# Optimization experiments

Hardware: AMD Instinct MI355X
Metric: run time of the kernel (lower is better)

Reference implementation:

```python
import jax, jax.numpy as jnp
import numpy as np

N = 500000      # total nodes
B = 10000       # number of graphs
D = 256         # node_size == global_size
SLOPE = 0.01    # LeakyReLU negative slope (torch default)

def leaky_relu(x):
    return jnp.where(x >= 0, x, SLOPE * x)

def setup_inputs() -> dict:
    key = jax.random.key(0)
    ks = jax.random.split(key, 10)
    xg_old = jax.random.normal(ks[0], (B, D), dtype=jnp.float32)
    x = jax.random.normal(ks[1], (N, D), dtype=jnp.float32)
    batch = jnp.sort(jax.random.randint(ks[2], (N,), 0, B)).astype(jnp.int64)
    s = 1.0 / np.sqrt(D)
    W_gate = jax.random.uniform(ks[3], (D, 1), minval=-s, maxval=s, dtype=jnp.float32)
    b_gate = jax.random.uniform(ks[4], (1,), minval=-s, maxval=s, dtype=jnp.float32)
    W_feat = jax.random.uniform(ks[5], (D, D), minval=-s, maxval=s, dtype=jnp.float32)
    b_feat = jax.random.uniform(ks[6], (D,), minval=-s, maxval=s, dtype=jnp.float32)
    s2 = 1.0 / np.sqrt(2 * D)
    W_t = jax.random.uniform(ks[7], (2 * D, D), minval=-s2, maxval=s2, dtype=jnp.float32)
    b_t = jax.random.uniform(ks[8], (D,), minval=-s2, maxval=s2, dtype=jnp.float32)
    return {"xg_old": xg_old, "x": x, "batch": batch,
            "W_gate": W_gate, "b_gate": b_gate,
            "W_feat": W_feat, "b_feat": b_feat,
            "W_t": W_t, "b_t": b_t}

def reference(xg_old, x, batch, W_gate, b_gate, W_feat, b_feat, W_t, b_t):
    batch = batch.astype(jnp.int32)
    # AttentionalAggregation: per-graph softmax over gate scores, weighted sum of feats
    gate = x @ W_gate + b_gate                               # [N, 1]
    feat = leaky_relu(x @ W_feat + b_feat)                   # [N, D]
    m = jax.ops.segment_max(gate, batch, num_segments=B)     # [B, 1]
    g = jnp.exp(gate - m[batch])                             # stable exp
    s = jax.ops.segment_sum(g, batch, num_segments=B)        # [B, 1]
    alpha = g / s[batch]                                     # [N, 1]
    xg = jax.ops.segment_sum(alpha * feat, batch, num_segments=B)  # [B, D]
    # concat with old global state, transform, residual
    cat = jnp.concatenate([xg, xg_old], axis=1)              # [B, 2D]
    out = leaky_relu(cat @ W_t + b_t) + xg_old               # [B, D]
    return out
```

## Files before the change

kernel.cpp:

```cpp
#include <hip/hip_runtime.h>
#include <hip/hip_bf16.h>
#include <math.h>

#define D 256

typedef short v8s __attribute__((ext_vector_type(8)));
typedef float f32x4 __attribute__((ext_vector_type(4)));

__global__ void segstart_kernel(const int* __restrict__ batch, int* __restrict__ seg_start,
                                int N, int B) {
    int b = blockIdx.x * blockDim.x + threadIdx.x;
    if (b > B) return;
    int lo = 0, hi = N;
    while (lo < hi) {
        int mid = (lo + hi) >> 1;
        if (batch[mid] < b) lo = mid + 1; else hi = mid;
    }
    seg_start[b] = lo;
}

__global__ __launch_bounds__(256) void gate_kernel(const float* __restrict__ x,
                                                   const float* __restrict__ Wg,
                                                   const float* __restrict__ bg,
                                                   float* __restrict__ gate, int N) {
    int wave = threadIdx.x >> 6;
    int lane = threadIdx.x & 63;
    int n = blockIdx.x * 4 + wave;
    if (n >= N) return;
    const float4 xv = *(const float4*)(x + (size_t)n * D + lane * 4);
    const float4 wv = *(const float4*)(Wg + lane * 4);
    float d = xv.x * wv.x + xv.y * wv.y + xv.z * wv.z + xv.w * wv.w;
    #pragma unroll
    for (int off = 32; off > 0; off >>= 1) d += __shfl_down(d, off, 64);
    if (lane == 0) gate[n] = d + bg[0];
}

__global__ __launch_bounds__(256) void stats_kernel(const float* __restrict__ gate,
                                                    const int* __restrict__ seg_start,
                                                    float* __restrict__ mvec,
                                                    float* __restrict__ invs, int B) {
    int wid = blockIdx.x * 4 + (threadIdx.x >> 6);
    int lane = threadIdx.x & 63;
    if (wid >= B) return;
    int s0 = seg_start[wid], s1 = seg_start[wid + 1];
    float m = -INFINITY;
    for (int i = s0 + lane; i < s1; i += 64) m = fmaxf(m, gate[i]);
    #pragma unroll
    for (int off = 32; off > 0; off >>= 1) m = fmaxf(m, __shfl_xor(m, off, 64));
    float s = 0.f;
    for (int i = s0 + lane; i < s1; i += 64) s += __expf(gate[i] - m);
    #pragma unroll
    for (int off = 32; off > 0; off >>= 1) s += __shfl_xor(s, off, 64);
    if (lane == 0) { mvec[wid] = m; invs[wid] = (s > 0.f) ? 1.f / s : 0.f; }
}

__global__ void wconv_kernel(const float* __restrict__ Wf, unsigned short* __restrict__ Wb) {
    int idx = blockIdx.x * 256 + threadIdx.x;
    int k = idx >> 8, n = idx & 255;
    int n_tile = n >> 4, k_step = k >> 5;
    int lane = ((k >> 3) & 3) * 16 + (n & 15);
    int j = k & 7;
    int dst = (((n_tile * 8 + k_step) * 64) + lane) * 8 + j;
    Wb[dst] = __bfloat16_as_ushort(__float2bfloat16(Wf[k * 256 + n]));
}

__global__ __launch_bounds__(256) void feat_attn_kernel(
    const float* __restrict__ x, const unsigned short* __restrict__ Wb,
    const float* __restrict__ bfeat, const float* __restrict__ gate,
    const int* __restrict__ batch, const float* __restrict__ mvec,
    const float* __restrict__ invs, float* __restrict__ xg, int N) {

    __shared__ unsigned short feat_s[64 * 260];
    __shared__ float alpha_s[64];
    __shared__ int batch_s[64];

    const int tid = threadIdx.x;
    const int n0 = blockIdx.x * 64;
    const int cnt = min(64, N - n0);

    if (tid < 64) {
        if (tid < cnt) {
            int n = n0 + tid;
            int b = batch[n];
            batch_s[tid] = b;
            alpha_s[tid] = __expf(gate[n] - mvec[b]) * invs[b];
        } else { batch_s[tid] = -1; alpha_s[tid] = 0.f; }
    }

    const int w = tid >> 6, lane = tid & 63;
    const int mrow = lane & 15, q = lane >> 4;

    f32x4 acc[4][4];
    #pragma unroll
    for (int i = 0; i < 4; i++)
        #pragma unroll
        for (int j = 0; j < 4; j++) acc[i][j] = (f32x4){0.f, 0.f, 0.f, 0.f};

    size_t rowbase[4];
    #pragma unroll
    for (int rb = 0; rb < 4; rb++) {
        int r = n0 + rb * 16 + mrow;
        if (r > N - 1) r = N - 1;
        rowbase[rb] = (size_t)r * D + q * 8;
    }

    for (int ks = 0; ks < 8; ks++) {
        v8s a[4], bfr[4];
        #pragma unroll
        for (int rb = 0; rb < 4; rb++) {
            const float* p = x + rowbase[rb] + ks * 32;
            float4 f0 = *(const float4*)p;
            float4 f1 = *(const float4*)(p + 4);
            v8s v;
            v[0] = (short)__bfloat16_as_ushort(__float2bfloat16(f0.x));
            v[1] = (short)__bfloat16_as_ushort(__float2bfloat16(f0.y));
            v[2] = (short)__bfloat16_as_ushort(__float2bfloat16(f0.z));
            v[3] = (short)__bfloat16_as_ushort(__float2bfloat16(f0.w));
            v[4] = (short)__bfloat16_as_ushort(__float2bfloat16(f1.x));
            v[5] = (short)__bfloat16_as_ushort(__float2bfloat16(f1.y));
            v[6] = (short)__bfloat16_as_ushort(__float2bfloat16(f1.z));
            v[7] = (short)__bfloat16_as_ushort(__float2bfloat16(f1.w));
            a[rb] = v;
        }
        #pragma unroll
        for (int cb = 0; cb < 4; cb++) {
            int nt = w * 4 + cb;
            bfr[cb] = *(const v8s*)(Wb + (((size_t)nt * 8 + ks) * 64 + lane) * 8);
        }
        #pragma unroll
        for (int rb = 0; rb < 4; rb++)
            #pragma unroll
            for (int cb = 0; cb < 4; cb++)
                acc[rb][cb] = __builtin_amdgcn_mfma_f32_16x16x32_bf16(
                    a[rb], bfr[cb], acc[rb][cb], 0, 0, 0);
    }

    #pragma unroll
    for (int cb = 0; cb < 4; cb++) {
        int col = w * 64 + cb * 16 + mrow;
        float bias = bfeat[col];
        #pragma unroll
        for (int rb = 0; rb < 4; rb++) {
            #pragma unroll
            for (int reg = 0; reg < 4; reg++) {
                float y = acc[rb][cb][reg] + bias;
                y = (y >= 0.f) ? y : 0.01f * y;
                feat_s[(rb * 16 + q * 4 + reg) * 260 + col] =
                    __bfloat16_as_ushort(__float2bfloat16(y));
            }
        }
    }
    __syncthreads();

    float sum = 0.f;
    int cur = batch_s[0];
    for (int i = 0; i < cnt; i++) {
        int b = batch_s[i];
        if (b != cur) {
            atomicAdd(&xg[(size_t)cur * D + tid], sum);
            sum = 0.f; cur = b;
        }
        float y = __bfloat162float(__ushort_as_bfloat16(feat_s[i * 260 + tid]));
        sum = fmaf(alpha_s[i], y, sum);
    }
    atomicAdd(&xg[(size_t)cur * D + tid], sum);
}

__global__ __launch_bounds__(256) void out_kernel(
    const float* __restrict__ xg, const float* __restrict__ xg_old,
    const float* __restrict__ Wt, const float* __restrict__ bt,
    float* __restrict__ out) {
    const int t = threadIdx.x;
    const int r0 = blockIdx.x * 8;
    float acc[8];
    #pragma unroll
    for (int r = 0; r < 8; r++) acc[r] = 0.f;

    for (int k = 0; k < D; k++) {
        const float w = Wt[k * D + t];
        #pragma unroll
        for (int r = 0; r < 8; r++)
            acc[r] = fmaf(xg[(size_t)(r0 + r) * D + k], w, acc[r]);
    }
    for (int k = 0; k < D; k++) {
        const float w = Wt[(D + k) * D + t];
        #pragma unroll
        for (int r = 0; r < 8; r++)
            acc[r] = fmaf(xg_old[(size_t)(r0 + r) * D + k], w, acc[r]);
    }
    const float btt = bt[t];
    #pragma unroll
    for (int r = 0; r < 8; r++) {
        float y = acc[r] + btt;
        y = (y >= 0.f) ? y : 0.01f * y;
        out[(size_t)(r0 + r) * D + t] = y + xg_old[(size_t)(r0 + r) * D + t];
    }
}

extern "C" void kernel_launch(void* const* d_in, const int* in_sizes, int n_in,
                              void* d_out, int out_size, void* d_ws, size_t ws_size,
                              hipStream_t stream) {
    const float* xg_old = (const float*)d_in[0];
    const float* x      = (const float*)d_in[1];
    const int*   batch  = (const int*)d_in[2];
    const float* W_gate = (const float*)d_in[3];
    const float* b_gate = (const float*)d_in[4];
    const float* W_feat = (const float*)d_in[5];
    const float* b_feat = (const float*)d_in[6];
    const float* W_t    = (const float*)d_in[7];
    const float* b_t    = (const float*)d_in[8];
    float* out = (float*)d_out;

    const int N = in_sizes[1] / D;
    const int B = in_sizes[0] / D;

    char* ws = (char*)d_ws;
    int*            seg_start = (int*)ws;
    float*          gate      = (float*)(ws + 0x10000);
    float*          mvec      = (float*)(ws + 0x220000);
    float*          invs      = (float*)(ws + 0x230000);
    unsigned short* Wb        = (unsigned short*)(ws + 0x240000);
    float*          xg        = (float*)(ws + 0x280000);

    segstart_kernel<<<(B + 1 + 255) / 256, 256, 0, stream>>>(batch, seg_start, N, B);
    gate_kernel<<<(N + 3) / 4, 256, 0, stream>>>(x, W_gate, b_gate, gate, N);
    stats_kernel<<<(B + 3) / 4, 256, 0, stream>>>(gate, seg_start, mvec, invs, B);
    wconv_kernel<<<256, 256, 0, stream>>>(W_feat, Wb);
    hipMemsetAsync(xg, 0, (size_t)B * D * sizeof(float), stream);
    feat_attn_kernel<<<(N + 63) / 64, 256, 0, stream>>>(
        x, Wb, b_feat, gate, batch, mvec, invs, xg, N);
    out_kernel<<<B / 8, 256, 0, stream>>>(xg, xg_old, W_t, b_t, out);
}
```

Measured before the change: 1.106 ms.

## Pre-convert x to bf16 in gate pass and use MFMA for output transform

The gate kernel becomes a grid-stride loop that also writes a bf16 copy of x, so the feature GEMM can read half the bytes instead of re-reading fp32 x. The output transform is rewritten to use bf16 MFMA, working on a bf16 concat buffer and a pre-swizzled W_t, replacing the scalar FMA loop. This adds an extra write of a bf16 copy of x (N*D*2 bytes) plus conversion kernels, and lowers the precision of the final GEMM. Both paths are gated on workspace size, with the old code kept as a fallback.

New measurement: 988.0 us. 10.7% less time.

```diff
diff --git a/kernel.cpp b/kernel.cpp
--- a/kernel.cpp
+++ b/kernel.cpp
@@ -6,6 +6,10 @@
 
 typedef short v8s __attribute__((ext_vector_type(8)));
 typedef float f32x4 __attribute__((ext_vector_type(4)));
+
+__device__ __forceinline__ unsigned short f2b(float f) {
+    return __bfloat16_as_ushort(__float2bfloat16(f));
+}
 
 __global__ void segstart_kernel(const int* __restrict__ batch, int* __restrict__ seg_start,
                                 int N, int B) {
@@ -19,20 +23,27 @@
     seg_start[b] = lo;
 }
 
-__global__ __launch_bounds__(256) void gate_kernel(const float* __restrict__ x,
-                                                   const float* __restrict__ Wg,
-                                                   const float* __restrict__ bg,
-                                                   float* __restrict__ gate, int N) {
-    int wave = threadIdx.x >> 6;
-    int lane = threadIdx.x & 63;
-    int n = blockIdx.x * 4 + wave;
-    if (n >= N) return;
-    const float4 xv = *(const float4*)(x + (size_t)n * D + lane * 4);
+template<bool CONV>
+__global__ __launch_bounds__(256) void gate_conv_kernel(
+    const float* __restrict__ x, const float* __restrict__ Wg,
+    const float* __restrict__ bg, float* __restrict__ gate,
+    unsigned short* __restrict__ xb16, int N) {
+    const int lane = threadIdx.x & 63;
+    const int wid = blockIdx.x * 4 + (threadIdx.x >> 6);
+    const int nw = gridDim.x * 4;
     const float4 wv = *(const float4*)(Wg + lane * 4);
-    float d = xv.x * wv.x + xv.y * wv.y + xv.z * wv.z + xv.w * wv.w;
-    #pragma unroll
-    for (int off = 32; off > 0; off >>= 1) d += __shfl_down(d, off, 64);
-    if (lane == 0) gate[n] = d + bg[0];
+    const float bgv = bg[0];
+    for (int n = wid; n < N; n += nw) {
+        const float4 xv = *(const float4*)(x + (size_t)n * D + lane * 4);
+        if (CONV) {
+            ushort4 h = { f2b(xv.x), f2b(xv.y), f2b(xv.z), f2b(xv.w) };
+            *(ushort4*)(xb16 + (size_t)n * D + lane * 4) = h;
+        }
+        float d = xv.x * wv.x + xv.y * wv.y + xv.z * wv.z + xv.w * wv.w;
+        #pragma unroll
+        for (int off = 32; off; off >>= 1) d += __shfl_xor(d, off, 64);
+        if (lane == 0) gate[n] = d + bgv;
+    }
 }
 
 __global__ __launch_bounds__(256) void stats_kernel(const float* __restrict__ gate,
@@ -54,18 +65,22 @@
     if (lane == 0) { mvec[wid] = m; invs[wid] = (s > 0.f) ? 1.f / s : 0.f; }
 }
 
-__global__ void wconv_kernel(const float* __restrict__ Wf, unsigned short* __restrict__ Wb) {
+__global__ void wconv_kernel(const float* __restrict__ Wf, unsigned short* __restrict__ Wb,
+                             int K) {
     int idx = blockIdx.x * 256 + threadIdx.x;
     int k = idx >> 8, n = idx & 255;
-    int n_tile = n >> 4, k_step = k >> 5;
+    if (k >= K) return;
+    int n_tile = n >> 4, k_step = k >> 5, ksteps = K >> 5;
     int lane = ((k >> 3) & 3) * 16 + (n & 15);
     int j = k & 7;
-    int dst = (((n_tile * 8 + k_step) * 64) + lane) * 8 + j;
-    Wb[dst] = __bfloat16_as_ushort(__float2bfloat16(Wf[k * 256 + n]));
-}
-
+    int dst = (((n_tile * ksteps + k_step) * 64) + lane) * 8 + j;
+    Wb[dst] = f2b(Wf[k * 256 + n]);
+}
+
+template<bool BF16IN>
 __global__ __launch_bounds__(256) void feat_attn_kernel(
-    const float* __restrict__ x, const unsigned short* __restrict__ Wb,
+    const float* __restrict__ x, const unsigned short* __restrict__ xb16,
+    const unsigned short* __restrict__ Wb,
     const float* __restrict__ bfeat, const float* __restrict__ gate,
     const int* __restrict__ batch, const float* __restrict__ mvec,
     const float* __restrict__ invs, float* __restrict__ xg, int N) {
@@ -108,19 +123,19 @@
         v8s a[4], bfr[4];
         #pragma unroll
         for (int rb = 0; rb < 4; rb++) {
-            const float* p = x + rowbase[rb] + ks * 32;
-            float4 f0 = *(const float4*)p;
-            float4 f1 = *(const float4*)(p + 4);
-            v8s v;
-            v[0] = (short)__bfloat16_as_ushort(__float2bfloat16(f0.x));
-            v[1] = (short)__bfloat16_as_ushort(__float2bfloat16(f0.y));
-            v[2] = (short)__bfloat16_as_ushort(__float2bfloat16(f0.z));
-            v[3] = (short)__bfloat16_as_ushort(__float2bfloat16(f0.w));
-            v[4] = (short)__bfloat16_as_ushort(__float2bfloat16(f1.x));
-            v[5] = (short)__bfloat16_as_ushort(__float2bfloat16(f1.y));
-            v[6] = (short)__bfloat16_as_ushort(__float2bfloat16(f1.z));
-            v[7] = (short)__bfloat16_as_ushort(__float2bfloat16(f1.w));
-            a[rb] = v;
+            if (BF16IN) {
+                a[rb] = *(const v8s*)(xb16 + rowbase[rb] + ks * 32);
+            } else {
+                const float* p = x + rowbase[rb] + ks * 32;
+                float4 f0 = *(const float4*)p;
+                float4 f1 = *(const float4*)(p + 4);
+                v8s v;
+                v[0] = (short)f2b(f0.x); v[1] = (short)f2b(f0.y);
+                v[2] = (short)f2b(f0.z); v[3] = (short)f2b(f0.w);
+                v[4] = (short)f2b(f1.x); v[5] = (short)f2b(f1.y);
+                v[6] = (short)f2b(f1.z); v[7] = (short)f2b(f1.w);
+                a[rb] = v;
+            }
         }
         #pragma unroll
         for (int cb = 0; cb < 4; cb++) {
@@ -145,8 +160,7 @@
             for (int reg = 0; reg < 4; reg++) {
                 float y = acc[rb][cb][reg] + bias;
                 y = (y >= 0.f) ? y : 0.01f * y;
-                feat_s[(rb * 16 + q * 4 + reg) * 260 + col] =
-                    __bfloat16_as_ushort(__float2bfloat16(y));
+                feat_s[(rb * 16 + q * 4 + reg) * 260 + col] = f2b(y);
             }
         }
     }
@@ -166,6 +180,76 @@
     atomicAdd(&xg[(size_t)cur * D + tid], sum);
 }
 
+__global__ void catconv_kernel(const float* __restrict__ xg, const float* __restrict__ xg_old,
+                               unsigned short* __restrict__ catb, int B) {
+    int idx = blockIdx.x * 256 + threadIdx.x;
+    if (idx >= B * 64) return;
+    int b = idx >> 6, c = (idx & 63) * 4;
+    float4 v1 = *(const float4*)(xg + (size_t)b * D + c);
+    float4 v2 = *(const float4*)(xg_old + (size_t)b * D + c);
+    ushort4 h1 = { f2b(v1.x), f2b(v1.y), f2b(v1.z), f2b(v1.w) };
+    ushort4 h2 = { f2b(v2.x), f2b(v2.y), f2b(v2.z), f2b(v2.w) };
+    *(ushort4*)(catb + (size_t)b * 512 + c) = h1;
+    *(ushort4*)(catb + (size_t)b * 512 + 256 + c) = h2;
+}
+
+__global__ __launch_bounds__(256) void out_mfma_kernel(
+    const unsigned short* __restrict__ catb, const unsigned short* __restrict__ Wtb,
+    const float* __restrict__ bt, const float* __restrict__ xg_old,
+    float* __restrict__ out, int B) {
+    const int tid = threadIdx.x;
+    const int w = tid >> 6, lane = tid & 63, mrow = lane & 15, q = lane >> 4;
+    const int r0 = blockIdx.x * 64;
+
+    f32x4 acc[4][4];
+    #pragma unroll
+    for (int i = 0; i < 4; i++)
+        #pragma unroll
+        for (int j = 0; j < 4; j++) acc[i][j] = (f32x4){0.f, 0.f, 0.f, 0.f};
+
+    size_t rowbase[4];
+    #pragma unroll
+    for (int rb = 0; rb < 4; rb++) {
+        int r = r0 + rb * 16 + mrow;
+        if (r > B - 1) r = B - 1;
+        rowbase[rb] = (size_t)r * 512 + q * 8;
+    }
+
+    for (int ks = 0; ks < 16; ks++) {
+        v8s a[4], bfr[4];
+        #pragma unroll
+        for (int rb = 0; rb < 4; rb++)
+            a[rb] = *(const v8s*)(catb + rowbase[rb] + ks * 32);
+        #pragma unroll
+        for (int cb = 0; cb < 4; cb++)
+            bfr[cb] = *(const v8s*)(Wtb + (((size_t)(w * 4 + cb) * 16 + ks) * 64 + lane) * 8);
+        #pragma unroll
+        for (int rb = 0; rb < 4; rb++)
+            #pragma unroll
+            for (int cb = 0; cb < 4; cb++)
+                acc[rb][cb] = __builtin_amdgcn_mfma_f32_16x16x32_bf16(
+                    a[rb], bfr[cb], acc[rb][cb], 0, 0, 0);
+    }
+
+    #pragma unroll
+    for (int cb = 0; cb < 4; cb++) {
+        int col = w * 64 + cb * 16 + mrow;
+        float bias = bt[col];
+        #pragma unroll
+        for (int rb = 0; rb < 4; rb++) {
+            #pragma unroll
+            for (int reg = 0; reg < 4; reg++) {
+                int row = r0 + rb * 16 + q * 4 + reg;
+                if (row < B) {
+                    float y = acc[rb][cb][reg] + bias;
+                    y = (y >= 0.f) ? y : 0.01f * y;
+                    out[(size_t)row * D + col] = y + xg_old[(size_t)row * D + col];
+                }
+            }
+        }
+    }
+}
+
 __global__ __launch_bounds__(256) void out_kernel(
     const float* __restrict__ xg, const float* __restrict__ xg_old,
     const float* __restrict__ Wt, const float* __restrict__ bt,
@@ -175,7 +259,6 @@
     float acc[8];
     #pragma unroll
     for (int r = 0; r < 8; r++) acc[r] = 0.f;
-
     for (int k = 0; k < D; k++) {
         const float w = Wt[k * D + t];
         #pragma unroll
@@ -220,14 +303,37 @@
     float*          mvec      = (float*)(ws + 0x220000);
     float*          invs      = (float*)(ws + 0x230000);
     unsigned short* Wb        = (unsigned short*)(ws + 0x240000);
-    float*          xg        = (float*)(ws + 0x280000);
+    unsigned short* Wtb       = (unsigned short*)(ws + 0x260000);
+    float*          xg        = (float*)(ws + 0x2A0000);
+    unsigned short* catb      = (unsigned short*)(ws + 0xCA0000);
+    unsigned short* xb16      = (unsigned short*)(ws + 0x16A0000);
+
+    const size_t need_full = 0x16A0000 + (size_t)N * D * 2;
+    const size_t need_mid  = 0x16A0000;
+    const bool full = ws_size >= need_full;
+    const bool mid  = ws_size >= need_mid;
 
     segstart_kernel<<<(B + 1 + 255) / 256, 256, 0, stream>>>(batch, seg_start, N, B);
-    gate_kernel<<<(N + 3) / 4, 256, 0, stream>>>(x, W_gate, b_gate, gate, N);
+    if (full)
+        gate_conv_kernel<true><<<2048, 256, 0, stream>>>(x, W_gate, b_gate, gate, xb16, N);
+    else
+        gate_conv_kernel<false><<<2048, 256, 0, stream>>>(x, W_gate, b_gate, gate, xb16, N);
     stats_kernel<<<(B + 3) / 4, 256, 0, stream>>>(gate, seg_start, mvec, invs, B);
-    wconv_kernel<<<256, 256, 0, stream>>>(W_feat, Wb);
+    wconv_kernel<<<256, 256, 0, stream>>>(W_feat, Wb, 256);
+    if (mid) wconv_kernel<<<512, 256, 0, stream>>>(W_t, Wtb, 512);
     hipMemsetAsync(xg, 0, (size_t)B * D * sizeof(float), stream);
-    feat_attn_kernel<<<(N + 63) / 64, 256, 0, stream>>>(
-        x, Wb, b_feat, gate, batch, mvec, invs, xg, N);
-    out_kernel<<<B / 8, 256, 0, stream>>>(xg, xg_old, W_t, b_t, out);
-}
+
+    if (full)
+        feat_attn_kernel<true><<<(N + 63) / 64, 256, 0, stream>>>(
+            x, xb16, Wb, b_feat, gate, batch, mvec, invs, xg, N);
+    else
+        feat_attn_kernel<false><<<(N + 63) / 64, 256, 0, stream>>>(
+            x, xb16, Wb, b_feat, gate, batch, mvec, invs, xg, N);
+
+    if (mid) {
+        catconv_kernel<<<(B * 64 + 255) / 256, 256, 0, stream>>>(xg, xg_old, catb, B);
+        out_mfma_kernel<<<(B + 63) / 64, 256, 0, stream>>>(catb, Wtb, b_t, xg_old, out, B);
+    } else {
+        out_kernel<<<B / 8, 256, 0, stream>>>(xg, xg_old, W_t, b_t, out);
+    }
+}
```
